# Performance work log

Hardware: AMD Instinct MI355X
Metric: run time of the kernel (lower is better)

The kernel has to match this reference:

```python
import jax, jax.numpy as jnp
import numpy as np

N = 100000   # nodes
E = 1000000  # edges
G = 2000     # graphs
ND = 64      # node_dim (== hidden_dim so per-layer params stack)
ED = 16      # edge_dim
HD = 64      # hidden_dim
L = 4        # num_layers


def setup_inputs() -> dict:
    key = jax.random.key(0)
    ks = jax.random.split(key, 16)
    s = 0.1  # param init scale
    return {
        "x": jax.random.normal(ks[0], (N, ND), jnp.float32),
        "edge_index": jax.random.randint(ks[1], (2, E), 0, N, jnp.int32),
        "edge_attr": jax.random.normal(ks[2], (E, ED), jnp.float32),
        "batch": jnp.sort(jax.random.randint(ks[3], (N,), 0, G, jnp.int32)),
        "t_cond": jax.random.uniform(ks[4], (G,), jnp.float32),
        # per-layer GINEConv params (stacked over L layers)
        "lin_e": jax.random.normal(ks[5], (L, ED, ND), jnp.float32) * s,  # edge_attr -> in_dim
        "W1": jax.random.normal(ks[6], (L, ND, HD), jnp.float32) * s,
        "b1": jnp.zeros((L, HD), jnp.float32),
        "W2": jax.random.normal(ks[7], (L, HD, HD), jnp.float32) * s,
        "b2": jnp.zeros((L, HD), jnp.float32),
        "eps": jnp.zeros((L,), jnp.float32),  # train_eps=True, init 0
        # head: Linear(HD+1 -> HD), ReLU, Linear(HD -> 1)
        "head_W1": jax.random.normal(ks[8], (HD + 1, HD), jnp.float32) * s,
        "head_b1": jnp.zeros((HD,), jnp.float32),
        "head_W2": jax.random.normal(ks[9], (HD, 1), jnp.float32) * s,
        "head_b2": jnp.zeros((1,), jnp.float32),
    }


def reference(x, edge_index, edge_attr, batch, t_cond,
              lin_e, W1, b1, W2, b2, eps,
              head_W1, head_b1, head_W2, head_b2):
    src = edge_index[0]  # x_j (message source)
    dst = edge_index[1]  # x_i (aggregation target)
    for l in range(L):
        # GINEConv: m_ij = ReLU(x_j + Lin(edge_attr)); aggr = sum_j m_ij
        e = edge_attr @ lin_e[l]                      # [E, ND]
        m = jax.nn.relu(x[src] + e)                   # gather + fuse
        aggr = jax.ops.segment_sum(m, dst, num_segments=N)  # scatter-add [N, ND]
        h = (1.0 + eps[l]) * x + aggr
        x = jax.nn.relu(h @ W1[l] + b1[l]) @ W2[l] + b2[l]  # nn_seq MLP
        x = jax.nn.relu(x)  # outer ReLU (dropout off at inference)
    # global mean pool over graphs
    sums = jax.ops.segment_sum(x, batch, num_segments=G)          # [G, HD]
    cnts = jax.ops.segment_sum(jnp.ones((N, 1), x.dtype), batch, num_segments=G)
    pooled = sums / jnp.maximum(cnts, 1.0)
    h = jnp.concatenate([pooled, t_cond[:, None].astype(x.dtype)], axis=-1)  # [G, HD+1]
    out = jax.nn.relu(h @ head_W1 + head_b1) @ head_W2 + head_b2             # [G, 1]
    return out
```

## Files before the change

kernel.cpp:

```cpp
#include <hip/hip_runtime.h>

#define NDIM 64
#define EDIM 16
#define SCAN_BS 256
#define SCAN_TILE 2048

typedef __attribute__((ext_vector_type(8))) short short8;
typedef __attribute__((ext_vector_type(4))) float f32x4;
typedef __attribute__((ext_vector_type(4))) float f4;
typedef __attribute__((ext_vector_type(4))) unsigned int u32x4;

#define AS4 __attribute__((address_space(4)))
__device__ inline const AS4 int* cs_i(const int* p) {
    return (const AS4 int*)(unsigned long long)p;
}
__device__ inline const AS4 u32x4* cs_u4(const unsigned int* p) {
    return (const AS4 u32x4*)(unsigned long long)p;
}

#define BF_LO(u) __uint_as_float((u) << 16)
#define BF_HI(u) __uint_as_float((u) & 0xffff0000u)

__device__ inline unsigned short f2bf_rne(float f) {
    unsigned int u = __float_as_uint(f);
    unsigned int r = u + 0x7FFFu + ((u >> 16) & 1u);
    return (unsigned short)(r >> 16);
}
__device__ inline float bf2f(unsigned short h) {
    return __uint_as_float(((unsigned int)h) << 16);
}
__device__ inline unsigned int pack2(float a, float b) {
    return (unsigned int)f2bf_rne(a) | ((unsigned int)f2bf_rne(b) << 16);
}
__device__ inline void cvt8(const float4 v0, const float4 v1, short8& hi, short8& lo) {
    float v[8] = {v0.x, v0.y, v0.z, v0.w, v1.x, v1.y, v1.z, v1.w};
#pragma unroll
    for (int j = 0; j < 8; ++j) {
        unsigned short h = f2bf_rne(v[j]);
        hi[j] = (short)h;
        lo[j] = (short)f2bf_rne(v[j] - bf2f(h));
    }
}


__global__ __launch_bounds__(256) void hist_kernel(const int* __restrict__ edge_index,
                                                   int* __restrict__ deg, int E) {
    int e = blockIdx.x * blockDim.x + threadIdx.x;
    if (e < E) atomicAdd(&deg[edge_index[E + e]], 1);
}

__global__ __launch_bounds__(SCAN_BS) void scan_tile_kernel(const int* __restrict__ deg,
                                                            int* __restrict__ excl,
                                                            int* __restrict__ tsum, int n) {
    __shared__ int sdata[SCAN_BS];
    int base = blockIdx.x * SCAN_TILE + threadIdx.x * 8;
    int v[8]; int s = 0;
#pragma unroll
    for (int j = 0; j < 8; ++j) { int idx = base + j; int val = (idx < n) ? deg[idx] : 0; v[j] = val; s += val; }
    sdata[threadIdx.x] = s;
    __syncthreads();
    for (int off = 1; off < SCAN_BS; off <<= 1) {
        int t = (threadIdx.x >= (unsigned)off) ? sdata[threadIdx.x - off] : 0;
        __syncthreads();
        sdata[threadIdx.x] += t;
        __syncthreads();
    }
    int incl = sdata[threadIdx.x];
    if (threadIdx.x == SCAN_BS - 1) tsum[blockIdx.x] = incl;
    int run = incl - s;
#pragma unroll
    for (int j = 0; j < 8; ++j) { int idx = base + j; if (idx < n) excl[idx] = run; run += v[j]; }
}

__global__ void scan_sums_kernel(int* tsum, int ntiles) {
    if (threadIdx.x == 0 && blockIdx.x == 0) {
        int run = 0;
        for (int i = 0; i < ntiles; ++i) { int t = tsum[i]; tsum[i] = run; run += t; }
    }
}

__global__ __launch_bounds__(256) void scan_add_kernel(int* __restrict__ rowptr,
                                                       const int* __restrict__ tsum,
                                                       int* __restrict__ fillc, int n, int E) {
    int i = blockIdx.x * blockDim.x + threadIdx.x;
    if (i < n) {
        int v = rowptr[i] + tsum[i / SCAN_TILE];
        rowptr[i] = v;
        fillc[i] = v;
    }
    if (i == 0) rowptr[n] = E;
}

__global__ __launch_bounds__(256) void fill_kernel(const int* __restrict__ edge_index,
                                                   int* __restrict__ fillc,
                                                   int* __restrict__ eids, int E) {
    int e = blockIdx.x * blockDim.x + threadIdx.x;
    if (e < E) {
        int d = edge_index[E + e];
        int pos = atomicAdd(&fillc[d], 1);
        __builtin_nontemporal_store(e, &eids[pos]);
    }
}

__global__ __launch_bounds__(256) void permute_kernel(const int* __restrict__ eids,
                                                      const int* __restrict__ edge_index,
                                                      const float4* __restrict__ ea,
                                                      u32x4* __restrict__ gea,
                                                      int* __restrict__ srcs,
                                                      int* __restrict__ gdst, int E) {
    int p = blockIdx.x * blockDim.x + threadIdx.x;
    if (p < E) {
        int e = eids[p];
        srcs[p] = edge_index[e];
        gdst[p] = edge_index[E + e];
        float4 r0 = ea[(size_t)e*4+0], r1 = ea[(size_t)e*4+1],
               r2 = ea[(size_t)e*4+2], r3 = ea[(size_t)e*4+3];
        u32x4 d0, d1;
        d0.x = pack2(r0.x, r0.y); d0.y = pack2(r0.z, r0.w);
        d0.z = pack2(r1.x, r1.y); d0.w = pack2(r1.z, r1.w);
        d1.x = pack2(r2.x, r2.y); d1.y = pack2(r2.z, r2.w);
        d1.z = pack2(r3.x, r3.y); d1.w = pack2(r3.z, r3.w);
        gea[(size_t)p*2+0] = d0; gea[(size_t)p*2+1] = d1;
    }
}

__global__ __launch_bounds__(256) void init_kernel(const float4* __restrict__ x,
                                                   float4* __restrict__ h,
                                                   unsigned short* __restrict__ xbf,
                                                   const float* __restrict__ eps, int n4) {
    float e1 = 1.0f + eps[0];
    int i = blockIdx.x * blockDim.x + threadIdx.x;
    int stride = gridDim.x * blockDim.x;
    for (; i < n4; i += stride) {
        float4 v = x[i];
        uint2 u;
        u.x = pack2(v.x, v.y);
        u.y = pack2(v.z, v.w);
        *(uint2*)(xbf + (size_t)i * 4) = u;
        v.x *= e1; v.y *= e1; v.z *= e1; v.w *= e1;
        h[i] = v;
    }
}

#define EDGE_FMA16B(m, U0, U1)                                          \
    m = fmaf(BF_LO(U0.x), le[ 0], m); m = fmaf(BF_HI(U0.x), le[ 1], m); \
    m = fmaf(BF_LO(U0.y), le[ 2], m); m = fmaf(BF_HI(U0.y), le[ 3], m); \
    m = fmaf(BF_LO(U0.z), le[ 4], m); m = fmaf(BF_HI(U0.z), le[ 5], m); \
    m = fmaf(BF_LO(U0.w), le[ 6], m); m = fmaf(BF_HI(U0.w), le[ 7], m); \
    m = fmaf(BF_LO(U1.x), le[ 8], m); m = fmaf(BF_HI(U1.x), le[ 9], m); \
    m = fmaf(BF_LO(U1.y), le[10], m); m = fmaf(BF_HI(U1.y), le[11], m); \
    m = fmaf(BF_LO(U1.z), le[12], m); m = fmaf(BF_HI(U1.z), le[13], m); \
    m = fmaf(BF_LO(U1.w), le[14], m); m = fmaf(BF_HI(U1.w), le[15], m);

#define EDGE_FMA16(m, A0, A1, A2, A3)                                   \
    m = fmaf(A0.x, le[ 0], m); m = fmaf(A0.y, le[ 1], m);               \
    m = fmaf(A0.z, le[ 2], m); m = fmaf(A0.w, le[ 3], m);               \
    m = fmaf(A1.x, le[ 4], m); m = fmaf(A1.y, le[ 5], m);               \
    m = fmaf(A1.z, le[ 6], m); m = fmaf(A1.w, le[ 7], m);               \
    m = fmaf(A2.x, le[ 8], m); m = fmaf(A2.y, le[ 9], m);               \
    m = fmaf(A2.z, le[10], m); m = fmaf(A2.w, le[11], m);               \
    m = fmaf(A3.x, le[12], m); m = fmaf(A3.y, le[13], m);               \
    m = fmaf(A3.z, le[14], m); m = fmaf(A3.w, le[15], m);


__global__ __launch_bounds__(256) void aggr_flat_kernel(
    const unsigned short* __restrict__ xbf, float* __restrict__ hacc,
    const int* __restrict__ srcs, const int* __restrict__ gdst,
    const unsigned int* __restrict__ gea,
    const float* __restrict__ lin_e, int layer, int E)
{
    const int lane = threadIdx.x & 63;
    float le[16];
    const float* lep = lin_e + (size_t)layer * EDIM * NDIM;
#pragma unroll
    for (int j = 0; j < EDIM; ++j) le[j] = lep[j * NDIM + lane];

    const AS4 int* sc = cs_i(srcs);
    const AS4 int* dc = cs_i(gdst);

    int w = (blockIdx.x * blockDim.x + threadIdx.x) >> 6;
    int W = (gridDim.x * blockDim.x) >> 6;
    int S = (E + W - 1) / W;
    int p    = __builtin_amdgcn_readfirstlane(w * S);
    int pend = __builtin_amdgcn_readfirstlane(min(E, p + S));
    if (p >= pend) return;

    float aggr = 0.0f;
    int dprev = dc[p];
    for (; p + 4 <= pend; p += 4) {
        int s0 = sc[p], s1 = sc[p+1], s2 = sc[p+2], s3 = sc[p+3];
        int d0 = dc[p], d1 = dc[p+1], d2 = dc[p+2], d3 = dc[p+3];
        float xs0 = bf2f(xbf[(size_t)s0 * NDIM + lane]);
        float xs1 = bf2f(xbf[(size_t)s1 * NDIM + lane]);
        float xs2 = bf2f(xbf[(size_t)s2 * NDIM + lane]);
        float xs3 = bf2f(xbf[(size_t)s3 * NDIM + lane]);
        const AS4 u32x4* ea = cs_u4(gea + (size_t)p * 8);
        u32x4 a0 = ea[0], a1 = ea[1], b0 = ea[2], b1 = ea[3];
        u32x4 c0 = ea[4], c1 = ea[5], g0 = ea[6], g1 = ea[7];
        float m0 = xs0, m1 = xs1, m2 = xs2, m3 = xs3;
        EDGE_FMA16B(m0, a0, a1)
        EDGE_FMA16B(m1, b0, b1)
        EDGE_FMA16B(m2, c0, c1)
        EDGE_FMA16B(m3, g0, g1)
        m0 = fmaxf(m0, 0.0f); m1 = fmaxf(m1, 0.0f);
        m2 = fmaxf(m2, 0.0f); m3 = fmaxf(m3, 0.0f);
        if (d3 == dprev) {
            aggr += (m0 + m1) + (m2 + m3);
        } else {
            if (d0 != dprev) { atomicAdd(&hacc[(size_t)dprev * NDIM + lane], aggr); aggr = 0.0f; dprev = d0; }
            aggr += m0;
            if (d1 != dprev) { atomicAdd(&hacc[(size_t)dprev * NDIM + lane], aggr); aggr = 0.0f; dprev = d1; }
            aggr += m1;
            if (d2 != dprev) { atomicAdd(&hacc[(size_t)dprev * NDIM + lane], aggr); aggr = 0.0f; dprev = d2; }
            aggr += m2;
            if (d3 != dprev) { atomicAdd(&hacc[(size_t)dprev * NDIM + lane], aggr); aggr = 0.0f; dprev = d3; }
            aggr += m3;
        }
    }
    for (; p < pend; ++p) {
        int s0 = sc[p];
        int d0 = dc[p];
        float xs0 = bf2f(xbf[(size_t)s0 * NDIM + lane]);
        const AS4 u32x4* ea = cs_u4(gea + (size_t)p * 8);
        u32x4 a0 = ea[0], a1 = ea[1];
        float m0 = xs0;
        EDGE_FMA16B(m0, a0, a1)
        if (d0 != dprev) { atomicAdd(&hacc[(size_t)dprev * NDIM + lane], aggr); aggr = 0.0f; dprev = d0; }
        aggr += fmaxf(m0, 0.0f);
    }
    atomicAdd(&hacc[(size_t)dprev * NDIM + lane], aggr);
}


__global__ __launch_bounds__(256) void mlp_mfma_kernel(
    float* __restrict__ h,
    const float* __restrict__ W1, const float* __restrict__ b1,
    const float* __restrict__ W2, const float* __restrict__ b2,
    const float* __restrict__ eps, int next_layer,
    float* __restrict__ hnext, unsigned short* __restrict__ xbf,
    int layer, int n_nodes)
{
    __shared__ unsigned short sW1hi[4096], sW1lo[4096], sW2hi[4096], sW2lo[4096];
    __shared__ float sY[4][16 * 64];

    const float* w1 = W1 + (size_t)layer * 4096;
    const float* w2 = W2 + (size_t)layer * 4096;
    for (int idx = threadIdx.x; idx < 4096; idx += 256) {
        int k = idx >> 6, n = idx & 63;
        int c = k >> 5, q = (k >> 3) & 3, j = k & 7;
        int fidx = ((c * 4 + q) * 64 + n) * 8 + j;
        float a = w1[idx];
        unsigned short hi = f2bf_rne(a);
        sW1hi[fidx] = hi;
        sW1lo[fidx] = f2bf_rne(a - bf2f(hi));
        float b = w2[idx];
        hi = f2bf_rne(b);
        sW2hi[fidx] = hi;
        sW2lo[fidx] = f2bf_rne(b - bf2f(hi));
    }
    __syncthreads();

    const int lane = threadIdx.x & 63;
    const int wid = threadIdx.x >> 6;
    const int m = lane & 15, q = lane >> 4;
    float* Y = sY[wid];

    const float e1n = (next_layer >= 0) ? (1.0f + eps[next_layer]) : 0.0f;

    float b1v[4], b2v[4];
#pragma unroll
    for (int nt = 0; nt < 4; ++nt) {
        b1v[nt] = b1[layer * 64 + m + nt * 16];
        b2v[nt] = b2[layer * 64 + m + nt * 16];
    }

    int tiles = (n_nodes + 15) >> 4;
    int gw = blockIdx.x * 4 + wid;
    int nw = gridDim.x * 4;
    for (int t = gw; t < tiles; t += nw) {
        int r0 = t << 4;
        int rA = r0 + m; if (rA > n_nodes - 1) rA = n_nodes - 1;
        const float* hrow = h + (size_t)rA * 64;

        short8 Ahi[2], Alo[2];
#pragma unroll
        for (int c = 0; c < 2; ++c) {
            const float4* hp = (const float4*)(hrow + c * 32 + q * 8);
            float4 v0 = hp[0], v1 = hp[1];
            cvt8(v0, v1, Ahi[c], Alo[c]);
        }

#pragma unroll
        for (int nt = 0; nt < 4; ++nt) {
            int col = m + nt * 16;
            f32x4 acc = {0.f, 0.f, 0.f, 0.f};
#pragma unroll
            for (int c = 0; c < 2; ++c) {
                short8 bh = *(const short8*)&sW1hi[((c * 4 + q) * 64 + col) * 8];
                short8 bl = *(const short8*)&sW1lo[((c * 4 + q) * 64 + col) * 8];
                acc = __builtin_amdgcn_mfma_f32_16x16x32_bf16(Ahi[c], bh, acc, 0, 0, 0);
                acc = __builtin_amdgcn_mfma_f32_16x16x32_bf16(Alo[c], bh, acc, 0, 0, 0);
                acc = __builtin_amdgcn_mfma_f32_16x16x32_bf16(Ahi[c], bl, acc, 0, 0, 0);
            }
#pragma unroll
            for (int i = 0; i < 4; ++i) {
                int row = q * 4 + i;
                float y = fmaxf(acc[i] + b1v[nt], 0.0f);
                int gran = ((m >> 2) + 4 * nt) ^ row;
                Y[(row << 6) + (gran << 2) + (m & 3)] = y;
            }
        }
        __asm__ volatile("s_waitcnt lgkmcnt(0)" ::: "memory");

        short8 Yhi[2], Ylo[2];
#pragma unroll
        for (int c = 0; c < 2; ++c) {
            int g0 = c * 8 + q * 2;
            float4 v0 = *(const float4*)&Y[(m << 6) + ((g0 ^ m) << 2)];
            float4 v1 = *(const float4*)&Y[(m << 6) + (((g0 + 1) ^ m) << 2)];
            cvt8(v0, v1, Yhi[c], Ylo[c]);
        }

#pragma unroll
        for (int nt = 0; nt < 4; ++nt) {
            int col = m + nt * 16;
            f32x4 acc = {0.f, 0.f, 0.f, 0.f};
#pragma unroll
            for (int c = 0; c < 2; ++c) {
                short8 bh = *(const short8*)&sW2hi[((c * 4 + q) * 64 + col) * 8];
                short8 bl = *(const short8*)&sW2lo[((c * 4 + q) * 64 + col) * 8];
                acc = __builtin_amdgcn_mfma_f32_16x16x32_bf16(Yhi[c], bh, acc, 0, 0, 0);
                acc = __builtin_amdgcn_mfma_f32_16x16x32_bf16(Ylo[c], bh, acc, 0, 0, 0);
                acc = __builtin_amdgcn_mfma_f32_16x16x32_bf16(Yhi[c], bl, acc, 0, 0, 0);
            }
#pragma unroll
            for (int i = 0; i < 4; ++i) {
                int row = r0 + q * 4 + i;
                if (row < n_nodes) {
                    float v = fmaxf(acc[i] + b2v[nt], 0.0f);
                    if (next_layer >= 0) {
                        hnext[(size_t)row * 64 + col] = e1n * v;
                        xbf[(size_t)row * 64 + col] = f2bf_rne(v);
                    } else {
                        h[(size_t)row * 64 + col] = v;
                    }
                }
            }
        }
    }
}

__global__ __launch_bounds__(256) void layer_kernel(
    const float* __restrict__ xin, float* __restrict__ xout,
    const int* __restrict__ rowptr, const int* __restrict__ eids,
    const int* __restrict__ edge_index,
    const float* __restrict__ edge_attr,
    const float* __restrict__ lin_e, const float* __restrict__ W1, const float* __restrict__ b1,
    const float* __restrict__ W2, const float* __restrict__ b2, const float* __restrict__ eps,
    int layer, int n_nodes, int E)
{
    __shared__ float s_W1[NDIM * NDIM];
    __shared__ float s_W2[NDIM * NDIM];
    const float* w1 = W1 + (size_t)layer * NDIM * NDIM;
    const float* w2 = W2 + (size_t)layer * NDIM * NDIM;
    for (int i = threadIdx.x; i < NDIM * NDIM; i += 256) { s_W1[i] = w1[i]; s_W2[i] = w2[i]; }
    const int lane = threadIdx.x & 63;
    float le[16];
    const float* lep = lin_e + (size_t)layer * EDIM * NDIM;
#pragma unroll
    for (int j = 0; j < EDIM; ++j) le[j] = lep[j * NDIM + lane];
    const float bb1 = b1[layer * NDIM + lane];
    const float bb2 = b2[layer * NDIM + lane];
    const float eps1 = 1.0f + eps[layer];
    __syncthreads();
    int gw = (blockIdx.x * blockDim.x + threadIdx.x) >> 6;
    int nw = (gridDim.x * blockDim.x) >> 6;
    for (int node = gw; node < n_nodes; node += nw) {
        int p0 = rowptr[node], p1 = rowptr[node + 1];
        float aggr = 0.0f;
        for (int p = p0; p < p1; ++p) {
            int e = eids[p];
            int s = edge_index[e];
            float xs = xin[(size_t)s * NDIM + lane];
            const float4* ea = (const float4*)(edge_attr + (size_t)e * EDIM);
            float4 a0 = ea[0], a1 = ea[1], a2 = ea[2], a3 = ea[3];
            float m0 = xs;
            EDGE_FMA16(m0, a0, a1, a2, a3)
            aggr += fmaxf(m0, 0.0f);
        }
        float h = fmaf(eps1, xin[(size_t)node * NDIM + lane], aggr);
        float o1 = bb1;
#pragma unroll 8
        for (int k = 0; k < NDIM; ++k) o1 = fmaf(__shfl(h, k), s_W1[k * NDIM + lane], o1);
        o1 = fmaxf(o1, 0.0f);
        float o2 = bb2;
#pragma unroll 8
        for (int k = 0; k < NDIM; ++k) o2 = fmaf(__shfl(o1, k), s_W2[k * NDIM + lane], o2);
        xout[(size_t)node * NDIM + lane] = fmaxf(o2, 0.0f);
    }
}


__global__ __launch_bounds__(256) void starts_kernel(const int* __restrict__ batch,
                                                     int* __restrict__ starts, int N, int G) {
    int g = blockIdx.x * blockDim.x + threadIdx.x;
    if (g <= G) {
        int lo = 0, hi = N;
        while (lo < hi) { int mid = (lo + hi) >> 1; if (batch[mid] < g) lo = mid + 1; else hi = mid; }
        starts[g] = lo;
    }
}

__global__ __launch_bounds__(256) void poolhead_kernel(const float* __restrict__ x,
                                                       const int* __restrict__ starts,
                                                       const float* __restrict__ t_cond,
                                                       const float* __restrict__ hW1,
                                                       const float* __restrict__ hb1,
                                                       const float* __restrict__ hW2,
                                                       const float* __restrict__ hb2,
                                                       float* __restrict__ out, int G) {
    __shared__ float sW1[(NDIM + 1) * NDIM];
    __shared__ float sb1[NDIM];
    __shared__ float sW2[NDIM];
    for (int i = threadIdx.x; i < (NDIM + 1) * NDIM; i += 256) sW1[i] = hW1[i];
    if (threadIdx.x < NDIM) { sb1[threadIdx.x] = hb1[threadIdx.x]; sW2[threadIdx.x] = hW2[threadIdx.x]; }
    __syncthreads();
    const int lane = threadIdx.x & 63;
    int gw = (blockIdx.x * blockDim.x + threadIdx.x) >> 6;
    int nw = (gridDim.x * blockDim.x) >> 6;
    for (int g = gw; g < G; g += nw) {
        int a = starts[g], b = starts[g + 1];
        float s0 = 0.0f, s1 = 0.0f, s2 = 0.0f, s3 = 0.0f;
        int n = a;
        for (; n + 4 <= b; n += 4) {
            s0 += x[(size_t)n * NDIM + lane];
            s1 += x[(size_t)(n + 1) * NDIM + lane];
            s2 += x[(size_t)(n + 2) * NDIM + lane];
            s3 += x[(size_t)(n + 3) * NDIM + lane];
        }
        for (; n < b; ++n) s0 += x[(size_t)n * NDIM + lane];
        float c = fmaxf((float)(b - a), 1.0f);
        float p = ((s0 + s1) + (s2 + s3)) / c;
        float t = t_cond[g];
        float o1 = fmaf(t, sW1[NDIM * NDIM + lane], sb1[lane]);
#pragma unroll 8
        for (int k = 0; k < NDIM; ++k) o1 = fmaf(__shfl(p, k), sW1[k * NDIM + lane], o1);
        o1 = fmaxf(o1, 0.0f);
        float v = o1 * sW2[lane];
        for (int off = 32; off > 0; off >>= 1) v += __shfl_down(v, off);
        if (lane == 0) out[g] = v + hb2[0];
    }
}


extern "C" void kernel_launch(void* const* d_in, const int* in_sizes, int n_in,
                              void* d_out, int out_size, void* d_ws, size_t ws_size,
                              hipStream_t stream) {
    const float* x_in      = (const float*)d_in[0];
    const int*   edge_index= (const int*)  d_in[1];
    const float* edge_attr = (const float*)d_in[2];
    const int*   batch     = (const int*)  d_in[3];
    const float* t_cond    = (const float*)d_in[4];
    const float* lin_e     = (const float*)d_in[5];
    const float* W1        = (const float*)d_in[6];
    const float* b1        = (const float*)d_in[7];
    const float* W2        = (const float*)d_in[8];
    const float* b2        = (const float*)d_in[9];
    const float* eps       = (const float*)d_in[10];
    const float* hW1       = (const float*)d_in[11];
    const float* hb1       = (const float*)d_in[12];
    const float* hW2       = (const float*)d_in[13];
    const float* hb2       = (const float*)d_in[14];
    float* out = (float*)d_out;

    const int N = in_sizes[3];
    const int E = in_sizes[1] / 2;
    const int G = in_sizes[4];
    const int L = in_sizes[10];
    const int ntiles = (N + SCAN_TILE - 1) / SCAN_TILE;

    char* p = (char*)d_ws;
    auto alloc = [&](size_t bytes) { char* r = p; p += (bytes + 255) & ~(size_t)255; return r; };
    int*   rowptr = (int*)  alloc((size_t)(N + 1) * 4);
    int*   fillc  = (int*)  alloc((size_t)N * 4);
    int*   srcs   = (int*)  alloc((size_t)E * 4);
    int*   gdst   = (int*)  alloc((size_t)E * 4);
    int*   tsum   = (int*)  alloc((size_t)ntiles * 4);
    int*   starts = (int*)  alloc((size_t)(G + 1) * 4);
    float* bufA   = (float*)alloc((size_t)N * NDIM * 4);
    float* bufB   = (float*)alloc((size_t)N * NDIM * 4);
    unsigned short* xbf = (unsigned short*)alloc((size_t)N * NDIM * 2);
    size_t base_used = (size_t)(p - (char*)d_ws);
    unsigned int* gea = (unsigned int*)alloc((size_t)E * 8 * 4);
    bool use_gea = (base_used + (size_t)E * 8 * 4) <= ws_size
                   && (size_t)E * 4 <= (size_t)N * NDIM * 4;
    int* eids = (int*)bufA;

    hipMemsetAsync(fillc, 0, (size_t)N * 4, stream);
    hist_kernel<<<(E + 255) / 256, 256, 0, stream>>>(edge_index, fillc, E);
    scan_tile_kernel<<<ntiles, SCAN_BS, 0, stream>>>(fillc, rowptr, tsum, N);
    scan_sums_kernel<<<1, 64, 0, stream>>>(tsum, ntiles);
    scan_add_kernel<<<(N + 255) / 256, 256, 0, stream>>>(rowptr, tsum, fillc, N, E);
    fill_kernel<<<(E + 255) / 256, 256, 0, stream>>>(edge_index, fillc, eids, E);
    if (use_gea) {
        permute_kernel<<<(E + 255) / 256, 256, 0, stream>>>(eids, edge_index, (const float4*)edge_attr,
                                                            (u32x4*)gea, srcs, gdst, E);
    }
    starts_kernel<<<(G + 256) / 256, 256, 0, stream>>>(batch, starts, N, G);

    const int n4 = N * NDIM / 4;
    if (use_gea) {
        float* hacc  = bufA;
        float* other = bufB;
        init_kernel<<<2048, 256, 0, stream>>>((const float4*)x_in, (float4*)hacc, xbf, eps, n4);
        for (int l = 0; l < L; ++l) {
            aggr_flat_kernel<<<2048, 256, 0, stream>>>(xbf, hacc, srcs, gdst, gea, lin_e, l, E);
            int nl = (l + 1 < L) ? l + 1 : -1;
            mlp_mfma_kernel<<<1024, 256, 0, stream>>>(hacc, W1, b1, W2, b2,
                                                      eps, nl, other, xbf, l, N);
            if (nl >= 0) { float* t = hacc; hacc = other; other = t; }
        }
        poolhead_kernel<<<512, 256, 0, stream>>>(hacc, starts, t_cond, hW1, hb1, hW2, hb2, out, G);
    } else {
        const float* cur = x_in;
        float* work = bufB;
        for (int l = 0; l < L; ++l) {
            float* tgt = (l == 0) ? bufB : work;
            layer_kernel<<<1024, 256, 0, stream>>>(cur, tgt, rowptr, eids, edge_index,
                                                   edge_attr, lin_e, W1, b1, W2, b2, eps, l, N, E);
            cur = tgt;
            work = (tgt == bufA) ? bufB : bufA;
        }
        poolhead_kernel<<<512, 256, 0, stream>>>(cur, starts, t_cond, hW1, hb1, hW2, hb2, out, G);
    }
}
```

Before: 689.0 us.

## Replace per-node atomic CSR build with two-pass bucketed counting sort

Builds the dst-sorted edge order with a coarse two-pass bucket sort. Edges are first histogrammed and scattered into 512-node buckets using LDS-local atomics, then each bucket is sorted in shared memory by local node id. This replaces global per-node atomics in the hist and fill kernels, which are meant to be contended and scattered. It adds a serial single-thread scan and LDS capacity limits, and buckets larger than the LDS capacity fall back to unsorted order.

```diff
diff --git a/kernel.cpp b/kernel.cpp
--- a/kernel.cpp
+++ b/kernel.cpp
@@ -4,10 +4,13 @@
 #define EDIM 16
 #define SCAN_BS 256
 #define SCAN_TILE 2048
+#define BSHIFT 9
+#define NB_MAX 256
+#define P1_TILE 4096
+#define P2_CAP 8192
 
 typedef __attribute__((ext_vector_type(8))) short short8;
 typedef __attribute__((ext_vector_type(4))) float f32x4;
-typedef __attribute__((ext_vector_type(4))) float f4;
 typedef __attribute__((ext_vector_type(4))) unsigned int u32x4;
 
 #define AS4 __attribute__((address_space(4)))
@@ -39,6 +42,101 @@
         unsigned short h = f2bf_rne(v[j]);
         hi[j] = (short)h;
         lo[j] = (short)f2bf_rne(v[j] - bf2f(h));
+    }
+}
+
+
+__global__ __launch_bounds__(256) void bucket_hist_kernel(const int* __restrict__ edge_index,
+                                                          int* __restrict__ bhist, int E, int NB) {
+    __shared__ int lh[NB_MAX];
+    for (int i = threadIdx.x; i < NB; i += 256) lh[i] = 0;
+    __syncthreads();
+    int base = blockIdx.x * P1_TILE;
+    for (int i = threadIdx.x; i < P1_TILE; i += 256) {
+        int e = base + i;
+        if (e < E) atomicAdd(&lh[edge_index[E + e] >> BSHIFT], 1);
+    }
+    __syncthreads();
+    for (int i = threadIdx.x; i < NB; i += 256) if (lh[i]) atomicAdd(&bhist[i], lh[i]);
+}
+
+__global__ void bucket_scan_kernel(const int* __restrict__ bhist,
+                                   int* __restrict__ boff, int* __restrict__ bcur, int NB) {
+    if (threadIdx.x == 0 && blockIdx.x == 0) {
+        int run = 0;
+        for (int i = 0; i < NB; ++i) { boff[i] = run; bcur[i] = run; run += bhist[i]; }
+        boff[NB] = run;
+    }
+}
+
+__global__ __launch_bounds__(256) void bucket_scatter_kernel(const int* __restrict__ edge_index,
+                                                             int* __restrict__ bcur,
+                                                             int* __restrict__ eids, int E, int NB) {
+    __shared__ int lh[NB_MAX];
+    __shared__ int lbase[NB_MAX];
+    for (int i = threadIdx.x; i < NB; i += 256) lh[i] = 0;
+    __syncthreads();
+    int base = blockIdx.x * P1_TILE;
+    for (int i = threadIdx.x; i < P1_TILE; i += 256) {
+        int e = base + i;
+        if (e < E) atomicAdd(&lh[edge_index[E + e] >> BSHIFT], 1);
+    }
+    __syncthreads();
+    for (int i = threadIdx.x; i < NB; i += 256) {
+        int c = lh[i];
+        lbase[i] = c ? atomicAdd(&bcur[i], c) : 0;
+    }
+    __syncthreads();
+    for (int i = threadIdx.x; i < NB; i += 256) lh[i] = 0;
+    __syncthreads();
+    for (int i = threadIdx.x; i < P1_TILE; i += 256) {
+        int e = base + i;
+        if (e < E) {
+            int cb = edge_index[E + e] >> BSHIFT;
+            int pos = lbase[cb] + atomicAdd(&lh[cb], 1);
+            eids[pos] = e;
+        }
+    }
+}
+
+__global__ __launch_bounds__(256) void bucket_sort_kernel(const int* __restrict__ edge_index,
+                                                          int* __restrict__ eids,
+                                                          int* __restrict__ gdst,
+                                                          const int* __restrict__ boff, int E) {
+    __shared__ int leids[P2_CAP];
+    __shared__ unsigned short lloc[P2_CAP];
+    __shared__ int cnt[512];
+    __shared__ int offs[512];
+    int b = blockIdx.x;
+    int base = boff[b], n = boff[b + 1] - base;
+    int node0 = b << BSHIFT;
+    int nproc = min(n, P2_CAP);
+    for (int i = threadIdx.x; i < 512; i += 256) cnt[i] = 0;
+    __syncthreads();
+    for (int i = threadIdx.x; i < nproc; i += 256) {
+        int e = eids[base + i];
+        leids[i] = e;
+        int loc = edge_index[E + e] - node0;
+        lloc[i] = (unsigned short)loc;
+        atomicAdd(&cnt[loc], 1);
+    }
+    __syncthreads();
+    if (threadIdx.x == 0) {
+        int run = 0;
+        for (int i = 0; i < 512; ++i) { offs[i] = run; run += cnt[i]; }
+    }
+    __syncthreads();
+    for (int i = threadIdx.x; i < 512; i += 256) cnt[i] = 0;
+    __syncthreads();
+    for (int i = threadIdx.x; i < nproc; i += 256) {
+        int loc = lloc[i];
+        int pos = offs[loc] + atomicAdd(&cnt[loc], 1);
+        eids[base + pos] = leids[i];
+        gdst[base + pos] = node0 + loc;
+    }
+    for (int i = P2_CAP + threadIdx.x; i < n; i += 256) {
+        int e = eids[base + i];
+        gdst[base + i] = edge_index[E + e];
     }
 }
 
@@ -98,7 +196,7 @@
     if (e < E) {
         int d = edge_index[E + e];
         int pos = atomicAdd(&fillc[d], 1);
-        __builtin_nontemporal_store(e, &eids[pos]);
+        eids[pos] = e;
     }
 }
 
@@ -478,6 +576,7 @@
     const int G = in_sizes[4];
     const int L = in_sizes[10];
     const int ntiles = (N + SCAN_TILE - 1) / SCAN_TILE;
+    const int NB = (N + (1 << BSHIFT) - 1) >> BSHIFT;
 
     char* p = (char*)d_ws;
     auto alloc = [&](size_t bytes) { char* r = p; p += (bytes + 255) & ~(size_t)255; return r; };
@@ -486,6 +585,9 @@
     int*   srcs   = (int*)  alloc((size_t)E * 4);
     int*   gdst   = (int*)  alloc((size_t)E * 4);
     int*   tsum   = (int*)  alloc((size_t)ntiles * 4);
+    int*   bhist  = (int*)  alloc((size_t)NB * 4);
+    int*   boff   = (int*)  alloc((size_t)(NB + 1) * 4);
+    int*   bcur   = (int*)  alloc((size_t)NB * 4);
     int*   starts = (int*)  alloc((size_t)(G + 1) * 4);
     float* bufA   = (float*)alloc((size_t)N * NDIM * 4);
     float* bufB   = (float*)alloc((size_t)N * NDIM * 4);
@@ -494,14 +596,25 @@
     unsigned int* gea = (unsigned int*)alloc((size_t)E * 8 * 4);
     bool use_gea = (base_used + (size_t)E * 8 * 4) <= ws_size
                    && (size_t)E * 4 <= (size_t)N * NDIM * 4;
+    bool fast_sort = use_gea && (NB <= NB_MAX);
     int* eids = (int*)bufA;
 
-    hipMemsetAsync(fillc, 0, (size_t)N * 4, stream);
-    hist_kernel<<<(E + 255) / 256, 256, 0, stream>>>(edge_index, fillc, E);
-    scan_tile_kernel<<<ntiles, SCAN_BS, 0, stream>>>(fillc, rowptr, tsum, N);
-    scan_sums_kernel<<<1, 64, 0, stream>>>(tsum, ntiles);
-    scan_add_kernel<<<(N + 255) / 256, 256, 0, stream>>>(rowptr, tsum, fillc, N, E);
-    fill_kernel<<<(E + 255) / 256, 256, 0, stream>>>(edge_index, fillc, eids, E);
+    const int p1_blocks = (E + P1_TILE - 1) / P1_TILE;
+
+    if (fast_sort) {
+        hipMemsetAsync(bhist, 0, (size_t)NB * 4, stream);
+        bucket_hist_kernel<<<p1_blocks, 256, 0, stream>>>(edge_index, bhist, E, NB);
+        bucket_scan_kernel<<<1, 64, 0, stream>>>(bhist, boff, bcur, NB);
+        bucket_scatter_kernel<<<p1_blocks, 256, 0, stream>>>(edge_index, bcur, eids, E, NB);
+        bucket_sort_kernel<<<NB, 256, 0, stream>>>(edge_index, eids, gdst, boff, E);
+    } else {
+        hipMemsetAsync(fillc, 0, (size_t)N * 4, stream);
+        hist_kernel<<<(E + 255) / 256, 256, 0, stream>>>(edge_index, fillc, E);
+        scan_tile_kernel<<<ntiles, SCAN_BS, 0, stream>>>(fillc, rowptr, tsum, N);
+        scan_sums_kernel<<<1, 64, 0, stream>>>(tsum, ntiles);
+        scan_add_kernel<<<(N + 255) / 256, 256, 0, stream>>>(rowptr, tsum, fillc, N, E);
+        fill_kernel<<<(E + 255) / 256, 256, 0, stream>>>(edge_index, fillc, eids, E);
+    }
     if (use_gea) {
         permute_kernel<<<(E + 255) / 256, 256, 0, stream>>>(eids, edge_index, (const float4*)edge_attr,
                                                             (u32x4*)gea, srcs, gdst, E);
```

New measurement: 612.3 us. 11.1% less time.
